# Optimization experiments

Hardware: AMD Instinct MI355X
Metric: run time of the kernel (lower is better)

## Reference

```python
import jax, jax.numpy as jnp
import numpy as np

B, N, E = 1024, 156, 1564
C_IN, C_HID, C_OUT = 301, 128, 128
BN_EPS = 1e-5


def setup_inputs() -> dict:
    key = jax.random.key(0)
    ks = jax.random.split(key, 12)
    x = jax.random.normal(ks[0], (B, N, C_IN), dtype=jnp.float32)
    edge_index = jax.random.randint(ks[1], (2, E), 0, N, dtype=jnp.int64)
    # GCNConv linear weights (PyG lin has no bias; conv bias added after aggregation)
    W0 = jax.random.normal(ks[2], (C_IN, C_HID), dtype=jnp.float32) / np.sqrt(C_IN)
    b0 = jnp.zeros((C_HID,), dtype=jnp.float32)
    W1 = jax.random.normal(ks[3], (C_HID, C_HID), dtype=jnp.float32) / np.sqrt(C_HID)
    b1 = jnp.zeros((C_HID,), dtype=jnp.float32)
    W2 = jax.random.normal(ks[4], (C_HID, C_OUT), dtype=jnp.float32) / np.sqrt(C_HID)
    b2 = jnp.zeros((C_OUT,), dtype=jnp.float32)
    # BatchNorm affine params (eval mode: running_mean=0, running_var=1)
    bn_w0 = jax.random.uniform(ks[5], (C_HID,), dtype=jnp.float32, minval=0.5, maxval=1.5)
    bn_b0 = jax.random.normal(ks[6], (C_HID,), dtype=jnp.float32) * 0.1
    bn_w1 = jax.random.uniform(ks[7], (C_HID,), dtype=jnp.float32, minval=0.5, maxval=1.5)
    bn_b1 = jax.random.normal(ks[8], (C_HID,), dtype=jnp.float32) * 0.1
    return {"x": x, "edge_index": edge_index,
            "W0": W0, "b0": b0, "bn_w0": bn_w0, "bn_b0": bn_b0,
            "W1": W1, "b1": b1, "bn_w1": bn_w1, "bn_b1": bn_b1,
            "W2": W2, "b2": b2}


def _gcn_norm(edge_index, num_nodes):
    # add self-loops, compute symmetric normalization deg^-1/2[src]*deg^-1/2[dst]
    loops = jnp.tile(jnp.arange(num_nodes, dtype=edge_index.dtype)[None, :], (2, 1))
    ei = jnp.concatenate([edge_index, loops], axis=1)  # [2, E+N]
    row, col = ei[0], ei[1]
    deg = jnp.zeros((num_nodes,), dtype=jnp.float32).at[col].add(1.0)
    dinv = jnp.where(deg > 0, deg ** -0.5, 0.0)
    return row, col, dinv[row] * dinv[col]


def _gcn_conv(h, row, col, norm, W, b):
    # h: [B, N, Cin] -> [B, N, Cout]
    h = jnp.einsum('bnc,co->bno', h, W)
    msg = h[:, row, :] * norm[None, :, None]          # [B, E+N, Cout]
    out = jnp.zeros_like(h).at[:, col, :].add(msg)    # scatter-add to dst nodes
    return out + b


def _bn_eval(h, w, b):
    # eval-mode BatchNorm1d with running_mean=0, running_var=1
    return h * (w / jnp.sqrt(1.0 + BN_EPS)) + b


def reference(x, edge_index, W0, b0, bn_w0, bn_b0, W1, b1, bn_w1, bn_b1, W2, b2):
    n = x.shape[1]
    row, col, norm = _gcn_norm(edge_index, n)
    h = jax.nn.relu(_bn_eval(_gcn_conv(x, row, col, norm, W0, b0), bn_w0, bn_b0))
    h = jax.nn.relu(_bn_eval(_gcn_conv(h, row, col, norm, W1, b1), bn_w1, bn_b1))
    return _gcn_conv(h, row, col, norm, W2, b2)
```

## Files before the change

### kernel.cpp

```cpp
#include <hip/hip_runtime.h>

#define NN    156
#define NP    160
#define CN    128
#define K0    301
#define KP0   320
#define BATCH 1024

#define W0_OFF 0
#define W1_OFF (128 * KP0)
#define W2_OFF (128 * KP0 + 128 * 128)

typedef __attribute__((ext_vector_type(8))) short bf16x8;
typedef __attribute__((ext_vector_type(4))) float f32x4;

__device__ __align__(16) ushort g_WtH[128 * (KP0 + 128 + 128)];
__device__ __align__(16) ushort g_WtL[128 * (KP0 + 128 + 128)];
__device__ __align__(16) ushort g_AdjH[NP * NP];
__device__ __align__(16) ushort g_AdjL[NP * NP];

__device__ __forceinline__ ushort bf16_rne(float f) {
    union { float f; uint32_t u; } v; v.f = f;
    return (ushort)((v.u + 0x7FFFu + ((v.u >> 16) & 1u)) >> 16);
}
__device__ __forceinline__ float bf16_f(ushort h) {
    union { float f; uint32_t u; } v; v.u = ((uint32_t)h) << 16; return v.f;
}
__device__ __forceinline__ ushort bf16_trunc(float f) {
    union { float f; uint32_t u; } v; v.f = f;
    return (ushort)(v.u >> 16);
}

__global__ __launch_bounds__(256) void prep_wt(const int* __restrict__ ei, int E,
        const float* __restrict__ W0, const float* __restrict__ W1,
        const float* __restrict__ W2) {
    __shared__ float adjf[NP * NP];
    __shared__ int   cnt[NP];
    __shared__ float dinv_s[NP];
    const int t = threadIdx.x;
    if (blockIdx.x == 0) {
        for (int i = t; i < NP * NP; i += 256) adjf[i] = 0.f;
        for (int n = t; n < NP; n += 256) cnt[n] = (n < NN) ? 1 : 0;
        __syncthreads();
        for (int e = t; e < E; e += 256) atomicAdd(&cnt[ei[E + e]], 1);
        __syncthreads();
        for (int n = t; n < NP; n += 256)
            dinv_s[n] = (cnt[n] > 0) ? rsqrtf((float)cnt[n]) : 0.f;
        __syncthreads();
        for (int e = t; e < E; e += 256) {
            const int r = ei[e], c = ei[E + e];
            atomicAdd(&adjf[c * NP + r], dinv_s[r] * dinv_s[c]);
        }
        for (int n = t; n < NN; n += 256)
            atomicAdd(&adjf[n * NP + n], dinv_s[n] * dinv_s[n]);
        __syncthreads();
        for (int i = t; i < NP * NP; i += 256) {
            const float v = adjf[i];
            const ushort h = bf16_rne(v);
            g_AdjH[i] = h;
            g_AdjL[i] = bf16_trunc(v - bf16_f(h));
        }
    } else {
        const int id = (blockIdx.x - 1) * 256 + t;
        const float* W; int K, KP, woff, local;
        if (id < 128 * KP0)              { W = W0; K = K0;  KP = KP0; woff = W0_OFF; local = id; }
        else if (id < 128 * (KP0 + 128)) { W = W1; K = 128; KP = 128; woff = W1_OFF; local = id - 128 * KP0; }
        else                             { W = W2; K = 128; KP = 128; woff = W2_OFF; local = id - 128 * (KP0 + 128); }
        const int n = local & 127, k = local >> 7;
        const float f = (k < K) ? W[(size_t)k * CN + n] : 0.f;
        const ushort h = bf16_rne(f);
        g_WtH[woff + n * KP + k] = h;
        g_WtL[woff + n * KP + k] = bf16_trunc(f - bf16_f(h));
    }
}

__global__ __launch_bounds__(512, 4) void fused_all(
        const float* __restrict__ x,
        const float* __restrict__ cb0, const float* __restrict__ bw0, const float* __restrict__ bb0,
        const float* __restrict__ cb1, const float* __restrict__ bw1, const float* __restrict__ bb1,
        const float* __restrict__ cb2, float* __restrict__ out) {
    __shared__ __align__(16) uint8_t smem[81920];
    uint8_t* const pH = smem;
    uint8_t* const pL = smem + 40960;

    const int t = threadIdx.x;
    const int lane = t & 63, wave = t >> 6;
    const int quad = lane >> 4, l15 = lane & 15;
    const int rb = (wave >> 2) * 80;
    const int cbs = (wave & 3) * 32;
    const int ch0 = wave * 16;
    const size_t arow0 = (size_t)blockIdx.x * NN;

    f32x4 acc[5][2];
    f32x4 og[10];

    const int kp  = (t & 15) * 2;
    const int r0s = t >> 4;
    float sv0[5], sv1[5];

    auto stage_load = [&](int kt) {
        const int kk = kt * 32 + kp;
#pragma unroll
        for (int s = 0; s < 5; s++) {
            const int r  = r0s + s * 32;
            const int rc = (r < NN) ? r : (NN - 1);
            const size_t abase = (arow0 + rc) * (size_t)K0;
            sv0[s] = (kk < K0)     ? x[abase + kk]     : 0.f;
            sv1[s] = (kk + 1 < K0) ? x[abase + kk + 1] : 0.f;
        }
    };
    auto stage_write = [&](int buf) {
        const int segoff = buf * 10240 + (((kp >> 3) * NP) << 4) + (kp & 7) * 2;
#pragma unroll
        for (int s = 0; s < 5; s++) {
            const int r = r0s + s * 32;
            const int off = segoff + (r << 4);
            const ushort h0 = bf16_rne(sv0[s]), h1 = bf16_rne(sv1[s]);
            *(ushort2*)(pH + off) = make_ushort2(h0, h1);
            *(ushort2*)(pL + off) = make_ushort2(bf16_trunc(sv0[s] - bf16_f(h0)),
                                                 bf16_trunc(sv1[s] - bf16_f(h1)));
        }
    };

    auto gemm_l0_tile = [&](int kt, int buf) {
        bf16x8 bH[2], bL[2];
#pragma unroll
        for (int j = 0; j < 2; j++) {
            const int wi = W0_OFF + (cbs + j * 16 + l15) * KP0 + kt * 32 + quad * 8;
            bH[j] = *(const bf16x8*)&g_WtH[wi];
            bL[j] = *(const bf16x8*)&g_WtL[wi];
        }
#pragma unroll
        for (int i = 0; i < 5; i++) {
            const int off = buf * 10240 + ((quad * NP + rb + i * 16 + l15) << 4);
            const bf16x8 aH = *(const bf16x8*)(pH + off);
            const bf16x8 aL = *(const bf16x8*)(pL + off);
#pragma unroll
            for (int j = 0; j < 2; j++) {
                acc[i][j] = __builtin_amdgcn_mfma_f32_16x16x32_bf16(aH, bH[j], acc[i][j], 0, 0, 0);
                acc[i][j] = __builtin_amdgcn_mfma_f32_16x16x32_bf16(aH, bL[j], acc[i][j], 0, 0, 0);
                acc[i][j] = __builtin_amdgcn_mfma_f32_16x16x32_bf16(aL, bH[j], acc[i][j], 0, 0, 0);
            }
        }
    };

    auto gemm_h = [&](int woff) {
#pragma unroll
        for (int i = 0; i < 5; i++)
#pragma unroll
            for (int j = 0; j < 2; j++) acc[i][j] = (f32x4){0.f, 0.f, 0.f, 0.f};
        for (int kt = 0; kt < 4; kt++) {
            bf16x8 bH[2], bL[2];
#pragma unroll
            for (int j = 0; j < 2; j++) {
                const int wi = woff + (cbs + j * 16 + l15) * CN + kt * 32 + quad * 8;
                bH[j] = *(const bf16x8*)&g_WtH[wi];
                bL[j] = *(const bf16x8*)&g_WtL[wi];
            }
#pragma unroll
            for (int i = 0; i < 5; i++) {
                const int off = ((kt * 4 + quad) * NP + rb + i * 16 + l15) << 4;
                const bf16x8 aH = *(const bf16x8*)(pH + off);
                const bf16x8 aL = *(const bf16x8*)(pL + off);
#pragma unroll
                for (int j = 0; j < 2; j++) {
                    acc[i][j] = __builtin_amdgcn_mfma_f32_16x16x32_bf16(aH, bH[j], acc[i][j], 0, 0, 0);
                    acc[i][j] = __builtin_amdgcn_mfma_f32_16x16x32_bf16(aH, bL[j], acc[i][j], 0, 0, 0);
                    acc[i][j] = __builtin_amdgcn_mfma_f32_16x16x32_bf16(aL, bH[j], acc[i][j], 0, 0, 0);
                }
            }
        }
    };

    auto write_tT = [&]() {
#pragma unroll
        for (int i = 0; i < 5; i++)
#pragma unroll
            for (int j = 0; j < 2; j++) {
                const int ch = cbs + j * 16 + l15;
                const int s0 = rb + i * 16 + quad * 4;
                const int off = (((s0 >> 3) * CN + ch) << 4) + (s0 & 7) * 2;
                ushort4 hs, ls;
#pragma unroll
                for (int rg = 0; rg < 4; rg++) {
                    const float v = acc[i][j][rg];
                    const ushort h = bf16_rne(v);
                    (&hs.x)[rg] = h;
                    (&ls.x)[rg] = bf16_trunc(v - bf16_f(h));
                }
                *(ushort4*)(pH + off) = hs;
                *(ushort4*)(pL + off) = ls;
            }
    };

    auto do_agg = [&]() {
#pragma unroll
        for (int nj = 0; nj < 10; nj++) og[nj] = (f32x4){0.f, 0.f, 0.f, 0.f};
        for (int k2 = 0; k2 < 5; k2++) {
            const int offA = ((k2 * 4 + quad) * CN + ch0 + l15) << 4;
            const bf16x8 tAH = *(const bf16x8*)(pH + offA);
            const bf16x8 tAL = *(const bf16x8*)(pL + offA);
#pragma unroll
            for (int nj = 0; nj < 10; nj++) {
                const int ai = (nj * 16 + l15) * NP + k2 * 32 + quad * 8;
                const bf16x8 gH = *(const bf16x8*)&g_AdjH[ai];
                const bf16x8 gL = *(const bf16x8*)&g_AdjL[ai];
                og[nj] = __builtin_amdgcn_mfma_f32_16x16x32_bf16(tAH, gH, og[nj], 0, 0, 0);
                og[nj] = __builtin_amdgcn_mfma_f32_16x16x32_bf16(tAH, gL, og[nj], 0, 0, 0);
                og[nj] = __builtin_amdgcn_mfma_f32_16x16x32_bf16(tAL, gH, og[nj], 0, 0, 0);
            }
        }
    };

    auto write_h = [&](const float* cb, const float* bw, const float* bb) {
        const float inv = rsqrtf(1.f + 1e-5f);
        const int c0 = ch0 + quad * 4;
        const float4 cbv = *(const float4*)&cb[c0];
        const float4 bwv = *(const float4*)&bw[c0];
        const float4 bbv = *(const float4*)&bb[c0];
#pragma unroll
        for (int nj = 0; nj < 10; nj++) {
            const int node = nj * 16 + l15;
            const int off = (((c0 >> 3) * NP + node) << 4) + (c0 & 7) * 2;
            ushort4 hs, ls;
#pragma unroll
            for (int rg = 0; rg < 4; rg++) {
                float v = og[nj][rg] + (&cbv.x)[rg];
                v = fmaxf(fmaf(v, (&bwv.x)[rg] * inv, (&bbv.x)[rg]), 0.f);
                const ushort h = bf16_rne(v);
                (&hs.x)[rg] = h;
                (&ls.x)[rg] = bf16_trunc(v - bf16_f(h));
            }
            *(ushort4*)(pH + off) = hs;
            *(ushort4*)(pL + off) = ls;
        }
    };

    auto write_out = [&](const float* cb) {
        const int c0 = ch0 + quad * 4;
        const float4 cbv = *(const float4*)&cb[c0];
#pragma unroll
        for (int nj = 0; nj < 10; nj++) {
            const int node = nj * 16 + l15;
            if (node < NN) {
                float4 o;
#pragma unroll
                for (int rg = 0; rg < 4; rg++)
                    (&o.x)[rg] = og[nj][rg] + (&cbv.x)[rg];
                *(float4*)&out[(arow0 + node) * CN + c0] = o;
            }
        }
    };

#pragma unroll
    for (int i = 0; i < 5; i++)
#pragma unroll
        for (int j = 0; j < 2; j++) acc[i][j] = (f32x4){0.f, 0.f, 0.f, 0.f};
    stage_load(0);
    stage_write(0);
    __syncthreads();
    for (int kt = 0; kt < 10; kt++) {
        if (kt < 9) stage_load(kt + 1);
        gemm_l0_tile(kt, kt & 1);
        if (kt < 9) stage_write((kt + 1) & 1);
        __syncthreads();
    }
    write_tT();
    __syncthreads();
    do_agg();
    __syncthreads();
    write_h(cb0, bw0, bb0);
    __syncthreads();
    gemm_h(W1_OFF);
    __syncthreads();
    write_tT();
    __syncthreads();
    do_agg();
    __syncthreads();
    write_h(cb1, bw1, bb1);
    __syncthreads();
    gemm_h(W2_OFF);
    __syncthreads();
    write_tT();
    __syncthreads();
    do_agg();
    write_out(cb2);
}

extern "C" void kernel_launch(void* const* d_in, const int* in_sizes, int n_in,
                              void* d_out, int out_size, void* d_ws, size_t ws_size,
                              hipStream_t stream) {
    const float* x    = (const float*)d_in[0];
    const int*   ei   = (const int*)  d_in[1];
    const float* W0   = (const float*)d_in[2];
    const float* b0   = (const float*)d_in[3];
    const float* bnw0 = (const float*)d_in[4];
    const float* bnb0 = (const float*)d_in[5];
    const float* W1   = (const float*)d_in[6];
    const float* b1   = (const float*)d_in[7];
    const float* bnw1 = (const float*)d_in[8];
    const float* bnb1 = (const float*)d_in[9];
    const float* W2   = (const float*)d_in[10];
    const float* b2   = (const float*)d_in[11];
    float* out = (float*)d_out;

    const int E = in_sizes[1] / 2;

    prep_wt<<<289, 256, 0, stream>>>(ei, E, W0, W1, W2);
    fused_all<<<BATCH, 512, 0, stream>>>(x, b0, bnw0, bnb0,
                                         b1, bnw1, bnb1, b2, out);
}
```

Measured before the change: 541.7 us.

## Use 4-wave blocks with larger per-wave tiles, register prefetch and folded BN scale

```diff
diff --git a/kernel.cpp b/kernel.cpp
--- a/kernel.cpp
+++ b/kernel.cpp
@@ -20,20 +20,23 @@
 __device__ __align__(16) ushort g_AdjL[NP * NP];
 
 __device__ __forceinline__ ushort bf16_rne(float f) {
-    union { float f; uint32_t u; } v; v.f = f;
-    return (ushort)((v.u + 0x7FFFu + ((v.u >> 16) & 1u)) >> 16);
+    return __builtin_bit_cast(ushort, (__bf16)f);
 }
 __device__ __forceinline__ float bf16_f(ushort h) {
-    union { float f; uint32_t u; } v; v.u = ((uint32_t)h) << 16; return v.f;
-}
-__device__ __forceinline__ ushort bf16_trunc(float f) {
-    union { float f; uint32_t u; } v; v.f = f;
-    return (ushort)(v.u >> 16);
+    return __builtin_bit_cast(float, (uint32_t)h << 16);
+}
+__device__ __forceinline__ ushort bf16_lo(float f, ushort h) {
+    return (ushort)(__builtin_bit_cast(uint32_t, f - bf16_f(h)) >> 16);
+}
+
+__device__ __forceinline__ void barrier_lgkm() {
+    asm volatile("s_waitcnt lgkmcnt(0)\n\ts_barrier" ::: "memory");
 }
 
 __global__ __launch_bounds__(256) void prep_wt(const int* __restrict__ ei, int E,
         const float* __restrict__ W0, const float* __restrict__ W1,
-        const float* __restrict__ W2) {
+        const float* __restrict__ W2, const float* __restrict__ bw0,
+        const float* __restrict__ bw1) {
     __shared__ float adjf[NP * NP];
     __shared__ int   cnt[NP];
     __shared__ float dinv_s[NP];
@@ -58,7 +61,7 @@
             const float v = adjf[i];
             const ushort h = bf16_rne(v);
             g_AdjH[i] = h;
-            g_AdjL[i] = bf16_trunc(v - bf16_f(h));
+            g_AdjL[i] = bf16_lo(v, h);
         }
     } else {
         const int id = (blockIdx.x - 1) * 256 + t;
@@ -67,14 +70,18 @@
         else if (id < 128 * (KP0 + 128)) { W = W1; K = 128; KP = 128; woff = W1_OFF; local = id - 128 * KP0; }
         else                             { W = W2; K = 128; KP = 128; woff = W2_OFF; local = id - 128 * (KP0 + 128); }
         const int n = local & 127, k = local >> 7;
-        const float f = (k < K) ? W[(size_t)k * CN + n] : 0.f;
+        const float inv = rsqrtf(1.f + 1e-5f);
+        float s = 1.f;
+        if (woff == W0_OFF) s = bw0[n] * inv;
+        else if (woff == W1_OFF) s = bw1[n] * inv;
+        const float f = (k < K) ? W[(size_t)k * CN + n] * s : 0.f;
         const ushort h = bf16_rne(f);
         g_WtH[woff + n * KP + k] = h;
-        g_WtL[woff + n * KP + k] = bf16_trunc(f - bf16_f(h));
+        g_WtL[woff + n * KP + k] = bf16_lo(f, h);
     }
 }
 
-__global__ __launch_bounds__(512, 4) void fused_all(
+__global__ __launch_bounds__(256, 2) void fused_all(
         const float* __restrict__ x,
         const float* __restrict__ cb0, const float* __restrict__ bw0, const float* __restrict__ bb0,
         const float* __restrict__ cb1, const float* __restrict__ bw1, const float* __restrict__ bb1,
@@ -86,23 +93,24 @@
     const int t = threadIdx.x;
     const int lane = t & 63, wave = t >> 6;
     const int quad = lane >> 4, l15 = lane & 15;
-    const int rb = (wave >> 2) * 80;
-    const int cbs = (wave & 3) * 32;
-    const int ch0 = wave * 16;
+    const int wr = (wave >> 1) * 80;
+    const int wc = (wave & 1) * 64;
+    const int ac = (wave & 1) * 64;
+    const int ad = (wave >> 1) * 80;
     const size_t arow0 = (size_t)blockIdx.x * NN;
 
-    f32x4 acc[5][2];
-    f32x4 og[10];
+    f32x4 acc[5][4];
+    f32x4 og[4][5];
 
     const int kp  = (t & 15) * 2;
     const int r0s = t >> 4;
-    float sv0[5], sv1[5];
+    float sv0[10], sv1[10];
 
     auto stage_load = [&](int kt) {
         const int kk = kt * 32 + kp;
 #pragma unroll
-        for (int s = 0; s < 5; s++) {
-            const int r  = r0s + s * 32;
+        for (int s = 0; s < 10; s++) {
+            const int r  = r0s + s * 16;
             const int rc = (r < NN) ? r : (NN - 1);
             const size_t abase = (arow0 + rc) * (size_t)K0;
             sv0[s] = (kk < K0)     ? x[abase + kk]     : 0.f;
@@ -112,34 +120,43 @@
     auto stage_write = [&](int buf) {
         const int segoff = buf * 10240 + (((kp >> 3) * NP) << 4) + (kp & 7) * 2;
 #pragma unroll
-        for (int s = 0; s < 5; s++) {
-            const int r = r0s + s * 32;
-            const int off = segoff + (r << 4);
+        for (int s = 0; s < 10; s++) {
+            const int off = segoff + ((r0s + s * 16) << 4);
             const ushort h0 = bf16_rne(sv0[s]), h1 = bf16_rne(sv1[s]);
             *(ushort2*)(pH + off) = make_ushort2(h0, h1);
-            *(ushort2*)(pL + off) = make_ushort2(bf16_trunc(sv0[s] - bf16_f(h0)),
-                                                 bf16_trunc(sv1[s] - bf16_f(h1)));
-        }
-    };
-
-    auto gemm_l0_tile = [&](int kt, int buf) {
-        bf16x8 bH[2], bL[2];
-#pragma unroll
-        for (int j = 0; j < 2; j++) {
-            const int wi = W0_OFF + (cbs + j * 16 + l15) * KP0 + kt * 32 + quad * 8;
-            bH[j] = *(const bf16x8*)&g_WtH[wi];
-            bL[j] = *(const bf16x8*)&g_WtL[wi];
-        }
+            *(ushort2*)(pL + off) = make_ushort2(bf16_lo(sv0[s], h0), bf16_lo(sv1[s], h1));
+        }
+    };
+
+    bf16x8 wbH[2][4], wbL[2][4];
+    auto loadW = [&](int woff, int KP, int kt, int sl) {
+#pragma unroll
+        for (int j = 0; j < 4; j++) {
+            const int wi = woff + (wc + j * 16 + l15) * KP + kt * 32 + quad * 8;
+            wbH[sl][j] = *(const bf16x8*)&g_WtH[wi];
+            wbL[sl][j] = *(const bf16x8*)&g_WtL[wi];
+        }
+    };
+
+    bf16x8 gjH[4], gjL[4];
+    auto adj_pf = [&](int step) {
+        const int k2 = step / 5, nj = step % 5;
+        const int ai = (ad + nj * 16 + l15) * NP + k2 * 32 + quad * 8;
+        gjH[step & 3] = *(const bf16x8*)&g_AdjH[ai];
+        gjL[step & 3] = *(const bf16x8*)&g_AdjL[ai];
+    };
+
+    auto gemm_l0_tile = [&](int buf, int sl) {
 #pragma unroll
         for (int i = 0; i < 5; i++) {
-            const int off = buf * 10240 + ((quad * NP + rb + i * 16 + l15) << 4);
+            const int off = buf * 10240 + ((quad * NP + wr + i * 16 + l15) << 4);
             const bf16x8 aH = *(const bf16x8*)(pH + off);
             const bf16x8 aL = *(const bf16x8*)(pL + off);
 #pragma unroll
-            for (int j = 0; j < 2; j++) {
-                acc[i][j] = __builtin_amdgcn_mfma_f32_16x16x32_bf16(aH, bH[j], acc[i][j], 0, 0, 0);
-                acc[i][j] = __builtin_amdgcn_mfma_f32_16x16x32_bf16(aH, bL[j], acc[i][j], 0, 0, 0);
-                acc[i][j] = __builtin_amdgcn_mfma_f32_16x16x32_bf16(aL, bH[j], acc[i][j], 0, 0, 0);
+            for (int j = 0; j < 4; j++) {
+                acc[i][j] = __builtin_amdgcn_mfma_f32_16x16x32_bf16(aH, wbH[sl][j], acc[i][j], 0, 0, 0);
+                acc[i][j] = __builtin_amdgcn_mfma_f32_16x16x32_bf16(aH, wbL[sl][j], acc[i][j], 0, 0, 0);
+                acc[i][j] = __builtin_amdgcn_mfma_f32_16x16x32_bf16(aL, wbH[sl][j], acc[i][j], 0, 0, 0);
             }
         }
     };
@@ -148,25 +165,20 @@
 #pragma unroll
         for (int i = 0; i < 5; i++)
 #pragma unroll
-            for (int j = 0; j < 2; j++) acc[i][j] = (f32x4){0.f, 0.f, 0.f, 0.f};
+            for (int j = 0; j < 4; j++) acc[i][j] = (f32x4){0.f, 0.f, 0.f, 0.f};
+#pragma unroll
         for (int kt = 0; kt < 4; kt++) {
-            bf16x8 bH[2], bL[2];
-#pragma unroll
-            for (int j = 0; j < 2; j++) {
-                const int wi = woff + (cbs + j * 16 + l15) * CN + kt * 32 + quad * 8;
-                bH[j] = *(const bf16x8*)&g_WtH[wi];
-                bL[j] = *(const bf16x8*)&g_WtL[wi];
-            }
+            if (kt < 3) loadW(woff, CN, kt + 1, (kt + 1) & 1);
 #pragma unroll
             for (int i = 0; i < 5; i++) {
-                const int off = ((kt * 4 + quad) * NP + rb + i * 16 + l15) << 4;
+                const int off = ((kt * 4 + quad) * NP + wr + i * 16 + l15) << 4;
                 const bf16x8 aH = *(const bf16x8*)(pH + off);
                 const bf16x8 aL = *(const bf16x8*)(pL + off);
 #pragma unroll
-                for (int j = 0; j < 2; j++) {
-                    acc[i][j] = __builtin_amdgcn_mfma_f32_16x16x32_bf16(aH, bH[j], acc[i][j], 0, 0, 0);
-                    acc[i][j] = __builtin_amdgcn_mfma_f32_16x16x32_bf16(aH, bL[j], acc[i][j], 0, 0, 0);
-                    acc[i][j] = __builtin_amdgcn_mfma_f32_16x16x32_bf16(aL, bH[j], acc[i][j], 0, 0, 0);
+                for (int j = 0; j < 4; j++) {
+                    acc[i][j] = __builtin_amdgcn_mfma_f32_16x16x32_bf16(aH, wbH[kt & 1][j], acc[i][j], 0, 0, 0);
+                    acc[i][j] = __builtin_amdgcn_mfma_f32_16x16x32_bf16(aH, wbL[kt & 1][j], acc[i][j], 0, 0, 0);
+                    acc[i][j] = __builtin_amdgcn_mfma_f32_16x16x32_bf16(aL, wbH[kt & 1][j], acc[i][j], 0, 0, 0);
                 }
             }
         }
@@ -176,9 +188,9 @@
 #pragma unroll
         for (int i = 0; i < 5; i++)
 #pragma unroll
-            for (int j = 0; j < 2; j++) {
-                const int ch = cbs + j * 16 + l15;
-                const int s0 = rb + i * 16 + quad * 4;
+            for (int j = 0; j < 4; j++) {
+                const int ch = wc + j * 16 + l15;
+                const int s0 = wr + i * 16 + quad * 4;
                 const int off = (((s0 >> 3) * CN + ch) << 4) + (s0 & 7) * 2;
                 ushort4 hs, ls;
 #pragma unroll
@@ -186,7 +198,7 @@
                     const float v = acc[i][j][rg];
                     const ushort h = bf16_rne(v);
                     (&hs.x)[rg] = h;
-                    (&ls.x)[rg] = bf16_trunc(v - bf16_f(h));
+                    (&ls.x)[rg] = bf16_lo(v, h);
                 }
                 *(ushort4*)(pH + off) = hs;
                 *(ushort4*)(pL + off) = ls;
@@ -195,59 +207,77 @@
 
     auto do_agg = [&]() {
 #pragma unroll
-        for (int nj = 0; nj < 10; nj++) og[nj] = (f32x4){0.f, 0.f, 0.f, 0.f};
+        for (int mi = 0; mi < 4; mi++)
+#pragma unroll
+            for (int nj = 0; nj < 5; nj++) og[mi][nj] = (f32x4){0.f, 0.f, 0.f, 0.f};
+#pragma unroll
         for (int k2 = 0; k2 < 5; k2++) {
-            const int offA = ((k2 * 4 + quad) * CN + ch0 + l15) << 4;
-            const bf16x8 tAH = *(const bf16x8*)(pH + offA);
-            const bf16x8 tAL = *(const bf16x8*)(pL + offA);
-#pragma unroll
-            for (int nj = 0; nj < 10; nj++) {
-                const int ai = (nj * 16 + l15) * NP + k2 * 32 + quad * 8;
-                const bf16x8 gH = *(const bf16x8*)&g_AdjH[ai];
-                const bf16x8 gL = *(const bf16x8*)&g_AdjL[ai];
-                og[nj] = __builtin_amdgcn_mfma_f32_16x16x32_bf16(tAH, gH, og[nj], 0, 0, 0);
-                og[nj] = __builtin_amdgcn_mfma_f32_16x16x32_bf16(tAH, gL, og[nj], 0, 0, 0);
-                og[nj] = __builtin_amdgcn_mfma_f32_16x16x32_bf16(tAL, gH, og[nj], 0, 0, 0);
+            bf16x8 taH[4], taL[4];
+#pragma unroll
+            for (int mi = 0; mi < 4; mi++) {
+                const int off = ((k2 * 4 + quad) * CN + ac + mi * 16 + l15) << 4;
+                taH[mi] = *(const bf16x8*)(pH + off);
+                taL[mi] = *(const bf16x8*)(pL + off);
+            }
+#pragma unroll
+            for (int nj = 0; nj < 5; nj++) {
+                const int step = k2 * 5 + nj, slot = step & 3;
+#pragma unroll
+                for (int mi = 0; mi < 4; mi++) {
+                    og[mi][nj] = __builtin_amdgcn_mfma_f32_16x16x32_bf16(taH[mi], gjH[slot], og[mi][nj], 0, 0, 0);
+                    og[mi][nj] = __builtin_amdgcn_mfma_f32_16x16x32_bf16(taH[mi], gjL[slot], og[mi][nj], 0, 0, 0);
+                    og[mi][nj] = __builtin_amdgcn_mfma_f32_16x16x32_bf16(taL[mi], gjH[slot], og[mi][nj], 0, 0, 0);
+                }
+                if (step + 4 < 25) adj_pf(step + 4);
             }
         }
     };
 
     auto write_h = [&](const float* cb, const float* bw, const float* bb) {
         const float inv = rsqrtf(1.f + 1e-5f);
-        const int c0 = ch0 + quad * 4;
-        const float4 cbv = *(const float4*)&cb[c0];
-        const float4 bwv = *(const float4*)&bw[c0];
-        const float4 bbv = *(const float4*)&bb[c0];
-#pragma unroll
-        for (int nj = 0; nj < 10; nj++) {
-            const int node = nj * 16 + l15;
-            const int off = (((c0 >> 3) * NP + node) << 4) + (c0 & 7) * 2;
-            ushort4 hs, ls;
-#pragma unroll
-            for (int rg = 0; rg < 4; rg++) {
-                float v = og[nj][rg] + (&cbv.x)[rg];
-                v = fmaxf(fmaf(v, (&bwv.x)[rg] * inv, (&bbv.x)[rg]), 0.f);
-                const ushort h = bf16_rne(v);
-                (&hs.x)[rg] = h;
-                (&ls.x)[rg] = bf16_trunc(v - bf16_f(h));
-            }
-            *(ushort4*)(pH + off) = hs;
-            *(ushort4*)(pL + off) = ls;
+#pragma unroll
+        for (int mi = 0; mi < 4; mi++) {
+            const int c0 = ac + mi * 16 + quad * 4;
+            const float4 cbv = *(const float4*)&cb[c0];
+            const float4 bwv = *(const float4*)&bw[c0];
+            const float4 bbv = *(const float4*)&bb[c0];
+            float cbf[4];
+#pragma unroll
+            for (int rg = 0; rg < 4; rg++)
+                cbf[rg] = fmaf((&cbv.x)[rg], (&bwv.x)[rg] * inv, (&bbv.x)[rg]);
+#pragma unroll
+            for (int nj = 0; nj < 5; nj++) {
+                const int node = ad + nj * 16 + l15;
+                const int off = (((c0 >> 3) * NP + node) << 4) + (c0 & 7) * 2;
+                ushort4 hs, ls;
+#pragma unroll
+                for (int rg = 0; rg < 4; rg++) {
+                    const float v = fmaxf(og[mi][nj][rg] + cbf[rg], 0.f);
+                    const ushort h = bf16_rne(v);
+                    (&hs.x)[rg] = h;
+                    (&ls.x)[rg] = bf16_lo(v, h);
+                }
+                *(ushort4*)(pH + off) = hs;
+                *(ushort4*)(pL + off) = ls;
+            }
         }
     };
 
     auto write_out = [&](const float* cb) {
-        const int c0 = ch0 + quad * 4;
-        const float4 cbv = *(const float4*)&cb[c0];
-#pragma unroll
-        for (int nj = 0; nj < 10; nj++) {
-            const int node = nj * 16 + l15;
-            if (node < NN) {
-                float4 o;
-#pragma unroll
-                for (int rg = 0; rg < 4; rg++)
-                    (&o.x)[rg] = og[nj][rg] + (&cbv.x)[rg];
-                *(float4*)&out[(arow0 + node) * CN + c0] = o;
+#pragma unroll
+        for (int mi = 0; mi < 4; mi++) {
+            const int c0 = ac + mi * 16 + quad * 4;
+            const float4 cbv = *(const float4*)&cb[c0];
+#pragma unroll
+            for (int nj = 0; nj < 5; nj++) {
+                const int node = ad + nj * 16 + l15;
+                if (node < NN) {
+                    float4 o;
+#pragma unroll
+                    for (int rg = 0; rg < 4; rg++)
+                        (&o.x)[rg] = og[mi][nj][rg] + (&cbv.x)[rg];
+                    *(float4*)&out[(arow0 + node) * CN + c0] = o;
+                }
             }
         }
     };
@@ -255,34 +285,42 @@
 #pragma unroll
     for (int i = 0; i < 5; i++)
 #pragma unroll
-        for (int j = 0; j < 2; j++) acc[i][j] = (f32x4){0.f, 0.f, 0.f, 0.f};
+        for (int j = 0; j < 4; j++) acc[i][j] = (f32x4){0.f, 0.f, 0.f, 0.f};
     stage_load(0);
     stage_write(0);
-    __syncthreads();
+    loadW(W0_OFF, KP0, 0, 0);
+    barrier_lgkm();
+#pragma unroll
     for (int kt = 0; kt < 10; kt++) {
         if (kt < 9) stage_load(kt + 1);
-        gemm_l0_tile(kt, kt & 1);
+        if (kt < 9) loadW(W0_OFF, KP0, kt + 1, (kt + 1) & 1);
+        gemm_l0_tile(kt & 1, kt & 1);
         if (kt < 9) stage_write((kt + 1) & 1);
-        __syncthreads();
+        barrier_lgkm();
     }
     write_tT();
-    __syncthreads();
+    adj_pf(0); adj_pf(1); adj_pf(2); adj_pf(3);
+    barrier_lgkm();
     do_agg();
-    __syncthreads();
+    barrier_lgkm();
     write_h(cb0, bw0, bb0);
-    __syncthreads();
+    loadW(W1_OFF, CN, 0, 0);
+    barrier_lgkm();
     gemm_h(W1_OFF);
-    __syncthreads();
+    barrier_lgkm();
     write_tT();
-    __syncthreads();
+    adj_pf(0); adj_pf(1); adj_pf(2); adj_pf(3);
+    barrier_lgkm();
     do_agg();
-    __syncthreads();
+    barrier_lgkm();
     write_h(cb1, bw1, bb1);
-    __syncthreads();
+    loadW(W2_OFF, CN, 0, 0);
+    barrier_lgkm();
     gemm_h(W2_OFF);
-    __syncthreads();
+    barrier_lgkm();
     write_tT();
-    __syncthreads();
+    adj_pf(0); adj_pf(1); adj_pf(2); adj_pf(3);
+    barrier_lgkm();
     do_agg();
     write_out(cb2);
 }
@@ -306,7 +344,7 @@
 
     const int E = in_sizes[1] / 2;
 
-    prep_wt<<<289, 256, 0, stream>>>(ei, E, W0, W1, W2);
-    fused_all<<<BATCH, 512, 0, stream>>>(x, b0, bnw0, bnb0,
+    prep_wt<<<289, 256, 0, stream>>>(ei, E, W0, W1, W2, bnw0, bnw1);
+    fused_all<<<BATCH, 256, 0, stream>>>(x, b0, bnw0, bnb0,
                                          b1, bnw1, bnb1, b2, out);
 }
```

Measured after the change: 448.5 us. 17.2% less time.
